# Kernel optimization log

Hardware: AMD Instinct MI355X
Metric: run time of the kernel (lower is better)

The kernel has to match this reference:

```python
import jax, jax.numpy as jnp
import numpy as np

B, S, D = 4, 2048, 512
H, DK = 8, 64
FFN = 2048
LEFT, CHUNK, RIGHT = 512, 128, 128
EPS = 1e-5


def _emformer_mask():
    # True = disallowed. Each query attends to its own chunk, LEFT keys before
    # the chunk start, and RIGHT keys after the chunk end.
    idx = jnp.arange(S)
    cs = (idx // CHUNK) * CHUNK                      # chunk start per query
    j = idx[None, :]
    allowed = (j >= cs[:, None] - LEFT) & (j < cs[:, None] + CHUNK + RIGHT)
    return jnp.broadcast_to(~allowed, (B, 1, S, S))


def _ln(x, g, b):
    m = jnp.mean(x, axis=-1, keepdims=True)
    v = jnp.var(x, axis=-1, keepdims=True)
    return (x - m) * jax.lax.rsqrt(v + EPS) * g + b


def setup_inputs() -> dict:
    key = jax.random.key(0)
    ks = jax.random.split(key, 8)
    w = lambda k, shp: jax.random.normal(k, shp, dtype=jnp.float32) * 0.02
    return {
        "x": jax.random.normal(ks[0], (B, S, D), dtype=jnp.float32),
        "mask": _emformer_mask(),
        "ln_in_g": jnp.ones((D,), jnp.float32), "ln_in_b": jnp.zeros((D,), jnp.float32),
        "wq": w(ks[1], (D, D)), "bq": jnp.zeros((D,), jnp.float32),
        "wk": w(ks[2], (D, D)), "bk": jnp.zeros((D,), jnp.float32),
        "wv": w(ks[3], (D, D)), "bv": jnp.zeros((D,), jnp.float32),
        "ln1_g": jnp.ones((D,), jnp.float32), "ln1_b": jnp.zeros((D,), jnp.float32),
        "w1": w(ks[4], (D, FFN)), "b1": jnp.zeros((FFN,), jnp.float32),
        "w2": w(ks[5], (FFN, D)), "b2": jnp.zeros((D,), jnp.float32),
        "ln2_g": jnp.ones((D,), jnp.float32), "ln2_b": jnp.zeros((D,), jnp.float32),
    }


def reference(x, mask, ln_in_g, ln_in_b, wq, bq, wk, bk, wv, bv,
              ln1_g, ln1_b, w1, b1, w2, b2, ln2_g, ln2_b):
    h = _ln(x, ln_in_g, ln_in_b)                                  # [B,S,D]
    q = (h @ wq + bq).reshape(B, S, H, DK).transpose(0, 2, 1, 3)   # [B,H,S,DK]
    k = (h @ wk + bk).reshape(B, S, H, DK).transpose(0, 2, 1, 3)
    v = (h @ wv + bv).reshape(B, S, H, DK).transpose(0, 2, 1, 3)
    scores = jnp.einsum("bhqd,bhkd->bhqk", q, k) / np.sqrt(DK).astype(np.float32)
    scores = jnp.where(mask, -jnp.inf, scores)
    probs = jax.nn.softmax(scores, axis=-1)
    probs = jnp.where(mask, 0.0, probs)                           # masked_fill after softmax
    out = jnp.einsum("bhqk,bhkd->bhqd", probs, v)
    out = out.transpose(0, 2, 1, 3).reshape(B, S, D)
    attn_out = out + h                                            # residual uses post-LN input
    o = _ln(attn_out, ln1_g, ln1_b)
    o = (o @ w1 + b1) @ w2 + b2 + attn_out                        # NOTE: no activation in source
    return _ln(o, ln2_g, ln2_b)
```

## Files before the change

kernel.cpp:

```cpp
#include <hip/hip_runtime.h>
#include <stdint.h>

#define B_ 4
#define S_ 2048
#define D_ 512
#define H_ 8
#define FFN_ 2048
#define M_ (B_*S_)

typedef unsigned short u16;
typedef __attribute__((ext_vector_type(8))) __bf16 bf16x8;
typedef __attribute__((ext_vector_type(8))) u16 u16x8;
typedef __attribute__((ext_vector_type(4))) float f32x4;

__device__ __forceinline__ u16 f2bf(float f) {
  uint32_t u = __builtin_bit_cast(uint32_t, f);
  u += 0x7FFFu + ((u >> 16) & 1u);
  return (u16)(u >> 16);
}
__device__ __forceinline__ bf16x8 ldfrag(const u16* p) {
  return __builtin_bit_cast(bf16x8, *(const u16x8*)p);
}
__device__ __forceinline__ void gld16(const void* g, void* l) {
  __builtin_amdgcn_global_load_lds(
      (const __attribute__((address_space(1))) void*)g,
      (__attribute__((address_space(3))) void*)l, 16, 0, 0);
}

__global__ __launch_bounds__(256)
void wtrans(const float* __restrict__ W, int K, int N, u16* __restrict__ Wt) {
  __shared__ float t[32][33];
  int n0 = blockIdx.x * 32, k0 = blockIdx.y * 32;
  int x = threadIdx.x, y = threadIdx.y;
#pragma unroll
  for (int r = 0; r < 4; r++) t[y + 8*r][x] = W[(size_t)(k0 + y + 8*r) * N + n0 + x];
  __syncthreads();
#pragma unroll
  for (int r = 0; r < 4; r++) Wt[(size_t)(n0 + y + 8*r) * K + k0 + x] = f2bf(t[x][y + 8*r]);
}

__global__ void bcat(const float* __restrict__ bq, const float* __restrict__ bk,
                     const float* __restrict__ bv, float* __restrict__ o) {
  int i = blockIdx.x * 256 + threadIdx.x;
  o[i] = i < 512 ? bq[i] : (i < 1024 ? bk[i - 512] : bv[i - 1024]);
}

template <bool OUT32, bool OUT16>
__global__ __launch_bounds__(128)
void ln_k(const float* __restrict__ x, const float* __restrict__ g,
          const float* __restrict__ bta, float* __restrict__ y32, u16* __restrict__ y16) {
  int row = blockIdx.x;
  int t = threadIdx.x;
  const float* xr = x + (size_t)row * 512;
  f32x4 v = *(const f32x4*)(xr + t * 4);
  float s = v.x + v.y + v.z + v.w;
  float s2 = v.x*v.x + v.y*v.y + v.z*v.z + v.w*v.w;
#pragma unroll
  for (int m = 32; m; m >>= 1) { s += __shfl_xor(s, m); s2 += __shfl_xor(s2, m); }
  __shared__ float p[4];
  int wv = t >> 6;
  if ((t & 63) == 0) { p[wv] = s; p[2 + wv] = s2; }
  __syncthreads();
  s = p[0] + p[1]; s2 = p[2] + p[3];
  float mean = s * (1.f / 512.f);
  float var = s2 * (1.f / 512.f) - mean * mean;
  float rs = rsqrtf(var + 1e-5f);
#pragma unroll
  for (int j = 0; j < 4; j++) {
    float o = (v[j] - mean) * rs * g[t*4 + j] + bta[t*4 + j];
    if constexpr (OUT32) y32[(size_t)row * 512 + t*4 + j] = o;
    if constexpr (OUT16) y16[(size_t)row * 512 + t*4 + j] = f2bf(o);
  }
}

template <int NTW, int NCOL, bool RESID, bool OUT32, bool OUT16>
__global__ __launch_bounds__(256)
void gemm_db(const u16* __restrict__ A, const u16* __restrict__ Bt,
             const float* __restrict__ bias, int K, int N,
             const float* __restrict__ resid, float* __restrict__ C32,
             u16* __restrict__ C16) {
  __shared__ __align__(16) u16 As[2][128 * 32];
  __shared__ __align__(16) u16 Bs[2][NTW * 1024];
  const int tid = threadIdx.x;
  const int wave = tid >> 6, lane = tid & 63;
  const int l15 = lane & 15, quad = lane >> 4;
  const int wm = wave >> 1, wn = wave & 1;

  const int lin = blockIdx.x;
  const int rpx = (M_ / 128) / 8;
  const int xcd = lin & 7, local = lin >> 3;
  const int row0 = (xcd * rpx + local / NCOL) * 128;
  const int col0 = (local % NCOL) * (NTW * 32);

  f32x4 acc[4][NTW];
#pragma unroll
  for (int i = 0; i < 4; i++)
#pragma unroll
    for (int j = 0; j < NTW; j++) acc[i][j] = (f32x4){0.f, 0.f, 0.f, 0.f};

  const int lr = lane >> 2;
  const int lc = ((lane & 3) ^ ((lane >> 3) & 3)) * 8;
  const u16* aG0 = A + (size_t)(row0 + (wave * 2) * 16 + lr) * K + lc;
  const u16* aG1 = A + (size_t)(row0 + (wave * 2 + 1) * 16 + lr) * K + lc;
  const int aO0 = (wave * 2) * 512 + lane * 8;
  const int aO1 = (wave * 2 + 1) * 512 + lane * 8;
  const u16* bG[NTW / 2];
  int bO[NTW / 2];
#pragma unroll
  for (int i = 0; i < NTW / 2; i++) {
    int ch = wave * (NTW / 2) + i;
    bG[i] = Bt + (size_t)(col0 + ch * 16 + lr) * K + lc;
    bO[i] = ch * 512 + lane * 8;
  }
  const int rsw = (l15 >> 1) & 3;

  gld16(aG0, &As[0][aO0]);
  gld16(aG1, &As[0][aO1]);
#pragma unroll
  for (int i = 0; i < NTW / 2; i++) gld16(bG[i], &Bs[0][bO[i]]);

  const int nIter = K >> 5;
  for (int it = 0; it < nIter; it++) {
    __syncthreads();
    const int cur = it & 1;
    if (it + 1 < nIter) {
      const int nxt = cur ^ 1;
      const int k = (it + 1) << 5;
      gld16(aG0 + k, &As[nxt][aO0]);
      gld16(aG1 + k, &As[nxt][aO1]);
#pragma unroll
      for (int i = 0; i < NTW / 2; i++) gld16(bG[i] + k, &Bs[nxt][bO[i]]);
    }
    bf16x8 af[4], bf[NTW];
#pragma unroll
    for (int mt = 0; mt < 4; mt++)
      af[mt] = ldfrag(&As[cur][(wm * 64 + mt * 16 + l15) * 32 + ((quad ^ rsw) * 8)]);
#pragma unroll
    for (int nt = 0; nt < NTW; nt++)
      bf[nt] = ldfrag(&Bs[cur][(wn * (NTW * 16) + nt * 16 + l15) * 32 + ((quad ^ rsw) * 8)]);
#pragma unroll
    for (int mt = 0; mt < 4; mt++)
#pragma unroll
      for (int nt = 0; nt < NTW; nt++)
        acc[mt][nt] = __builtin_amdgcn_mfma_f32_16x16x32_bf16(af[mt], bf[nt], acc[mt][nt], 0, 0, 0);
  }
#pragma unroll
  for (int mt = 0; mt < 4; mt++)
#pragma unroll
    for (int nt = 0; nt < NTW; nt++) {
      int n = col0 + wn * (NTW * 16) + nt * 16 + l15;
      float bv = bias[n];
#pragma unroll
      for (int r = 0; r < 4; r++) {
        int m = row0 + wm * 64 + mt * 16 + quad * 4 + r;
        float val = acc[mt][nt][r] + bv;
        if constexpr (RESID) val += resid[(size_t)m * N + n];
        if constexpr (OUT32) C32[(size_t)m * N + n] = val;
        if constexpr (OUT16) C16[(size_t)m * N + n] = f2bf(val);
      }
    }
}

__global__ __launch_bounds__(256)
void vtrans(const u16* __restrict__ qkv, u16* __restrict__ vt) {
  __shared__ u16 t[64][65];
  int s0 = blockIdx.x * 64, h = blockIdx.y, b = blockIdx.z;
  int x = threadIdx.x, y = threadIdx.y;
  const u16* src = qkv + (size_t)(b * 2048 + s0) * 1536 + 1024 + h * 64;
#pragma unroll
  for (int r = 0; r < 16; r++) { int s = y + 4*r; t[s][x] = src[(size_t)s * 1536 + x]; }
  __syncthreads();
  u16* dst = vt + (size_t)((b * 8 + h) * 64) * 2048 + s0;
#pragma unroll
  for (int r = 0; r < 16; r++) { int d = y + 4*r; dst[(size_t)d * 2048 + x] = t[x][d]; }
}

#define PSTR 136
__global__ __launch_bounds__(256)
void attn_k(const u16* __restrict__ qkv, const u16* __restrict__ vt,
            const float* __restrict__ hres, float* __restrict__ attn) {
  __shared__ __align__(16) u16 smem[8192 + 8192 + 128 * PSTR];
  u16* Ks = smem;
  u16* Vts = smem + 8192;
  u16* Ps = smem + 16384;
  u16* Qs = Ps;

  const int c = blockIdx.x, hh = blockIdx.y, b = blockIdx.z;
  const int s0 = c * 128;
  const int tid = threadIdx.x, wave = tid >> 6, lane = tid & 63;
  const int l15 = lane & 15, quad = lane >> 4;
  const int t_lo = (c > 4) ? c - 4 : 0;
  const int t_hi = (c + 2 < 16) ? c + 2 : 16;
  const int l7sw = l15 & 7;

  {
    const int cg = ((lane & 7) ^ (lane >> 3)) * 8;
    const int cp = (lane & 7) * 8;
#pragma unroll
    for (int q2 = 0; q2 < 4; q2++) {
      int r = wave * 32 + q2 * 8 + (lane >> 3);
      gld16(qkv + (size_t)(b * 2048 + s0 + r) * 1536 + hh * 64 + cg, Qs + r * 64 + cp);
    }
  }
  __syncthreads();
  bf16x8 qf[2][2];
#pragma unroll
  for (int qg = 0; qg < 2; qg++)
#pragma unroll
    for (int f = 0; f < 2; f++)
      qf[qg][f] = ldfrag(Qs + (qg * 64 + wave * 16 + l15) * 64 + (((f * 4 + quad) ^ l7sw) * 8));

  f32x4 accO[2][4];
#pragma unroll
  for (int qg = 0; qg < 2; qg++)
#pragma unroll
    for (int i = 0; i < 4; i++) accO[qg][i] = (f32x4){0.f, 0.f, 0.f, 0.f};
  float den[2][4] = {{0.f, 0.f, 0.f, 0.f}, {0.f, 0.f, 0.f, 0.f}};

  for (int kt = t_lo; kt < t_hi; ++kt) {
    __syncthreads();
    {
      const int cgk = ((lane & 7) ^ (lane >> 3)) * 8;
      const int cpk = (lane & 7) * 8;
#pragma unroll
      for (int q2 = 0; q2 < 4; q2++) {
        int r = wave * 32 + q2 * 8 + (lane >> 3);
        gld16(qkv + (size_t)(b * 2048 + kt * 128 + r) * 1536 + 512 + hh * 64 + cgk,
              Ks + r * 64 + cpk);
      }
      const int cpv = (lane & 15) * 8;
#pragma unroll
      for (int q2 = 0; q2 < 4; q2++) {
        int d = (wave * 4 + q2) * 4 + (lane >> 4);
        int cgv = ((lane & 8) | ((lane & 7) ^ (lane >> 4) ^ ((q2 & 1) << 2))) * 8;
        gld16(vt + (size_t)((b * 8 + hh) * 64 + d) * 2048 + kt * 128 + cgv,
              Vts + d * 128 + cpv);
      }
    }
    __syncthreads();

#pragma unroll
    for (int nt = 0; nt < 8; nt++) {
      bf16x8 kf0 = ldfrag(Ks + (nt * 16 + l15) * 64 + ((quad ^ l7sw) * 8));
      bf16x8 kf1 = ldfrag(Ks + (nt * 16 + l15) * 64 + (((4 + quad) ^ l7sw) * 8));
#pragma unroll
      for (int qg = 0; qg < 2; qg++) {
        f32x4 s4 = (f32x4){0.f, 0.f, 0.f, 0.f};
        s4 = __builtin_amdgcn_mfma_f32_16x16x32_bf16(qf[qg][0], kf0, s4, 0, 0, 0);
        s4 = __builtin_amdgcn_mfma_f32_16x16x32_bf16(qf[qg][1], kf1, s4, 0, 0, 0);
#pragma unroll
        for (int r = 0; r < 4; r++) {
          float pp = exp2f(s4[r] * (1.4426950408889634f * 0.125f));
          den[qg][r] += pp;
          Ps[(qg * 64 + wave * 16 + quad * 4 + r) * PSTR + nt * 16 + l15] = f2bf(pp);
        }
      }
    }
#pragma unroll
    for (int ki = 0; ki < 4; ki++) {
      bf16x8 pf[2];
#pragma unroll
      for (int qg = 0; qg < 2; qg++)
        pf[qg] = ldfrag(Ps + (qg * 64 + wave * 16 + l15) * PSTR + (ki * 4 + quad) * 8);
#pragma unroll
      for (int dt = 0; dt < 4; dt++) {
        int g = ki * 4 + quad;
        bf16x8 vf = ldfrag(Vts + (dt * 16 + l15) * 128 + (((g & 8) | ((g & 7) ^ l7sw)) * 8));
#pragma unroll
        for (int qg = 0; qg < 2; qg++)
          accO[qg][dt] = __builtin_amdgcn_mfma_f32_16x16x32_bf16(pf[qg], vf, accO[qg][dt], 0, 0, 0);
      }
    }
  }
#pragma unroll
  for (int qg = 0; qg < 2; qg++)
#pragma unroll
    for (int r = 0; r < 4; r++) {
      float d = den[qg][r];
      d += __shfl_xor(d, 1); d += __shfl_xor(d, 2);
      d += __shfl_xor(d, 4); d += __shfl_xor(d, 8);
      den[qg][r] = d;
    }
#pragma unroll
  for (int qg = 0; qg < 2; qg++)
#pragma unroll
    for (int dt = 0; dt < 4; dt++)
#pragma unroll
      for (int r = 0; r < 4; r++) {
        int m = s0 + qg * 64 + wave * 16 + quad * 4 + r;
        size_t idx = (size_t)(b * 2048 + m) * 512 + hh * 64 + dt * 16 + l15;
        attn[idx] = accO[qg][dt][r] / den[qg][r] + hres[idx];
      }
}

extern "C" void kernel_launch(void* const* d_in, const int* in_sizes, int n_in,
                              void* d_out, int out_size, void* d_ws, size_t ws_size,
                              hipStream_t stream) {
  (void)in_sizes; (void)n_in; (void)out_size; (void)ws_size;
  const float* x       = (const float*)d_in[0];
  const float* ln_in_g = (const float*)d_in[2];
  const float* ln_in_b = (const float*)d_in[3];
  const float* wq = (const float*)d_in[4];
  const float* bq = (const float*)d_in[5];
  const float* wk = (const float*)d_in[6];
  const float* bk = (const float*)d_in[7];
  const float* wv = (const float*)d_in[8];
  const float* bv = (const float*)d_in[9];
  const float* ln1_g = (const float*)d_in[10];
  const float* ln1_b = (const float*)d_in[11];
  const float* w1 = (const float*)d_in[12];
  const float* b1 = (const float*)d_in[13];
  const float* w2 = (const float*)d_in[14];
  const float* b2 = (const float*)d_in[15];
  const float* ln2_g = (const float*)d_in[16];
  const float* ln2_b = (const float*)d_in[17];

  char* ws = (char*)d_ws;
  size_t off = 0;
  auto alloc = [&](size_t bytes) {
    void* p = ws + off;
    off = (off + bytes + 255) & ~(size_t)255;
    return p;
  };
  u16*   wqkvt = (u16*)  alloc((size_t)1536 * 512 * 2);
  float* bqkv  = (float*)alloc(1536 * 4);
  u16*   w1t   = (u16*)  alloc((size_t)2048 * 512 * 2);
  u16*   w2t   = (u16*)  alloc((size_t)512 * 2048 * 2);
  float* h32   = (float*)alloc((size_t)M_ * 512 * 4);
  u16*   h16   = (u16*)  alloc((size_t)M_ * 512 * 2);
  u16*   qkv16 = (u16*)  alloc((size_t)M_ * 1536 * 2);
  u16*   vtb   = (u16*)  alloc((size_t)B_ * H_ * 64 * 2048 * 2);
  float* attn32= (float*)alloc((size_t)M_ * 512 * 4);
  float* out2  = h32;
  u16*   o16   = h16;
  u16*   f16b  = qkv16;

  wtrans<<<dim3(16, 16), dim3(32, 8), 0, stream>>>(wq, 512, 512, wqkvt);
  wtrans<<<dim3(16, 16), dim3(32, 8), 0, stream>>>(wk, 512, 512, wqkvt + (size_t)512 * 512);
  wtrans<<<dim3(16, 16), dim3(32, 8), 0, stream>>>(wv, 512, 512, wqkvt + (size_t)1024 * 512);
  wtrans<<<dim3(64, 16), dim3(32, 8), 0, stream>>>(w1, 512, 2048, w1t);
  wtrans<<<dim3(16, 64), dim3(32, 8), 0, stream>>>(w2, 2048, 512, w2t);
  bcat<<<6, 256, 0, stream>>>(bq, bk, bv, bqkv);

  ln_k<true, true><<<M_, 128, 0, stream>>>(x, ln_in_g, ln_in_b, h32, h16);
  gemm_db<4, 12, false, false, true><<<dim3(12 * 64), 256, 0, stream>>>(
      h16, wqkvt, bqkv, 512, 1536, nullptr, nullptr, qkv16);
  vtrans<<<dim3(32, 8, 4), dim3(64, 4), 0, stream>>>(qkv16, vtb);
  attn_k<<<dim3(16, 8, 4), 256, 0, stream>>>(qkv16, vtb, h32, attn32);
  ln_k<false, true><<<M_, 128, 0, stream>>>(attn32, ln1_g, ln1_b, nullptr, o16);
  gemm_db<4, 16, false, false, true><<<dim3(16 * 64), 256, 0, stream>>>(
      o16, w1t, b1, 512, 2048, nullptr, nullptr, f16b);
  gemm_db<2, 8, true, true, false><<<dim3(8 * 64), 256, 0, stream>>>(
      f16b, w2t, b2, 2048, 512, attn32, out2, nullptr);
  ln_k<true, false><<<M_, 128, 0, stream>>>(out2, ln2_g, ln2_b, (float*)d_out, nullptr);
}
```

Measured before the change: 296.2 us.

## Split attention into 64-row query tiles and split-K the final FFN GEMM

```diff
diff --git a/kernel.cpp b/kernel.cpp
--- a/kernel.cpp
+++ b/kernel.cpp
@@ -11,6 +11,7 @@
 typedef unsigned short u16;
 typedef __attribute__((ext_vector_type(8))) __bf16 bf16x8;
 typedef __attribute__((ext_vector_type(8))) u16 u16x8;
+typedef __attribute__((ext_vector_type(4))) u16 u16x4;
 typedef __attribute__((ext_vector_type(4))) float f32x4;
 
 __device__ __forceinline__ u16 f2bf(float f) {
@@ -45,14 +46,21 @@
   o[i] = i < 512 ? bq[i] : (i < 1024 ? bk[i - 512] : bv[i - 1024]);
 }
 
-template <bool OUT32, bool OUT16>
+template <bool OUT32, bool OUT16, bool SUM2>
 __global__ __launch_bounds__(128)
 void ln_k(const float* __restrict__ x, const float* __restrict__ g,
-          const float* __restrict__ bta, float* __restrict__ y32, u16* __restrict__ y16) {
+          const float* __restrict__ bta, float* __restrict__ y32,
+          u16* __restrict__ y16, const u16* __restrict__ x2) {
   int row = blockIdx.x;
   int t = threadIdx.x;
   const float* xr = x + (size_t)row * 512;
   f32x4 v = *(const f32x4*)(xr + t * 4);
+  if constexpr (SUM2) {
+    u16x4 p2 = *(const u16x4*)(x2 + (size_t)row * 512 + t * 4);
+#pragma unroll
+    for (int j = 0; j < 4; j++)
+      v[j] += __builtin_bit_cast(float, (uint32_t)p2[j] << 16);
+  }
   float s = v.x + v.y + v.z + v.w;
   float s2 = v.x*v.x + v.y*v.y + v.z*v.z + v.w*v.w;
 #pragma unroll
@@ -73,7 +81,7 @@
   }
 }
 
-template <int NTW, int NCOL, bool RESID, bool OUT32, bool OUT16>
+template <int NTW, int NCOL, int KSPLIT, bool RESID, bool OUT32, bool OUT16>
 __global__ __launch_bounds__(256)
 void gemm_db(const u16* __restrict__ A, const u16* __restrict__ Bt,
              const float* __restrict__ bias, int K, int N,
@@ -86,11 +94,19 @@
   const int l15 = lane & 15, quad = lane >> 4;
   const int wm = wave >> 1, wn = wave & 1;
 
-  const int lin = blockIdx.x;
+  int lin = blockIdx.x;
+  int kh = 0;
+  if constexpr (KSPLIT == 2) {
+    const int nblk = (M_ / 128) * NCOL;
+    kh = lin >= nblk;
+    lin -= kh * nblk;
+  }
   const int rpx = (M_ / 128) / 8;
   const int xcd = lin & 7, local = lin >> 3;
   const int row0 = (xcd * rpx + local / NCOL) * 128;
   const int col0 = (local % NCOL) * (NTW * 32);
+  const int klen = K / KSPLIT;
+  const int kstart = kh * klen;
 
   f32x4 acc[4][NTW];
 #pragma unroll
@@ -114,18 +130,18 @@
   }
   const int rsw = (l15 >> 1) & 3;
 
-  gld16(aG0, &As[0][aO0]);
-  gld16(aG1, &As[0][aO1]);
-#pragma unroll
-  for (int i = 0; i < NTW / 2; i++) gld16(bG[i], &Bs[0][bO[i]]);
-
-  const int nIter = K >> 5;
+  gld16(aG0 + kstart, &As[0][aO0]);
+  gld16(aG1 + kstart, &As[0][aO1]);
+#pragma unroll
+  for (int i = 0; i < NTW / 2; i++) gld16(bG[i] + kstart, &Bs[0][bO[i]]);
+
+  const int nIter = klen >> 5;
   for (int it = 0; it < nIter; it++) {
     __syncthreads();
     const int cur = it & 1;
     if (it + 1 < nIter) {
       const int nxt = cur ^ 1;
-      const int k = (it + 1) << 5;
+      const int k = kstart + ((it + 1) << 5);
       gld16(aG0 + k, &As[nxt][aO0]);
       gld16(aG1 + k, &As[nxt][aO1]);
 #pragma unroll
@@ -149,14 +165,21 @@
 #pragma unroll
     for (int nt = 0; nt < NTW; nt++) {
       int n = col0 + wn * (NTW * 16) + nt * 16 + l15;
-      float bv = bias[n];
+      float bv;
+      if constexpr (KSPLIT == 2) bv = (kh == 0) ? bias[n] : 0.f;
+      else bv = bias[n];
 #pragma unroll
       for (int r = 0; r < 4; r++) {
         int m = row0 + wm * 64 + mt * 16 + quad * 4 + r;
         float val = acc[mt][nt][r] + bv;
-        if constexpr (RESID) val += resid[(size_t)m * N + n];
-        if constexpr (OUT32) C32[(size_t)m * N + n] = val;
-        if constexpr (OUT16) C16[(size_t)m * N + n] = f2bf(val);
+        if constexpr (KSPLIT == 2) {
+          if (kh == 0) C32[(size_t)m * N + n] = val + resid[(size_t)m * N + n];
+          else C16[(size_t)m * N + n] = f2bf(val);
+        } else {
+          if constexpr (RESID) val += resid[(size_t)m * N + n];
+          if constexpr (OUT32) C32[(size_t)m * N + n] = val;
+          if constexpr (OUT16) C16[(size_t)m * N + n] = f2bf(val);
+        }
       }
     }
 }
@@ -179,14 +202,19 @@
 __global__ __launch_bounds__(256)
 void attn_k(const u16* __restrict__ qkv, const u16* __restrict__ vt,
             const float* __restrict__ hres, float* __restrict__ attn) {
-  __shared__ __align__(16) u16 smem[8192 + 8192 + 128 * PSTR];
+  __shared__ __align__(16) u16 smem[8192 + 8192 + 64 * PSTR];
   u16* Ks = smem;
   u16* Vts = smem + 8192;
   u16* Ps = smem + 16384;
   u16* Qs = Ps;
 
-  const int c = blockIdx.x, hh = blockIdx.y, b = blockIdx.z;
-  const int s0 = c * 128;
+  const int lin = blockIdx.x;
+  const int xcd = lin & 7, g = lin >> 3;
+  const int cq = g & 31;
+  const int bh = xcd * 4 + (g >> 5);
+  const int hh = bh & 7, b = bh >> 3;
+  const int c = cq >> 1;
+  const int s0 = cq * 64;
   const int tid = threadIdx.x, wave = tid >> 6, lane = tid & 63;
   const int l15 = lane & 15, quad = lane >> 4;
   const int t_lo = (c > 4) ? c - 4 : 0;
@@ -197,25 +225,24 @@
     const int cg = ((lane & 7) ^ (lane >> 3)) * 8;
     const int cp = (lane & 7) * 8;
 #pragma unroll
-    for (int q2 = 0; q2 < 4; q2++) {
-      int r = wave * 32 + q2 * 8 + (lane >> 3);
+    for (int q2 = 0; q2 < 2; q2++) {
+      int r = wave * 16 + q2 * 8 + (lane >> 3);
       gld16(qkv + (size_t)(b * 2048 + s0 + r) * 1536 + hh * 64 + cg, Qs + r * 64 + cp);
     }
   }
   __syncthreads();
-  bf16x8 qf[2][2];
-#pragma unroll
-  for (int qg = 0; qg < 2; qg++)
-#pragma unroll
-    for (int f = 0; f < 2; f++)
-      qf[qg][f] = ldfrag(Qs + (qg * 64 + wave * 16 + l15) * 64 + (((f * 4 + quad) ^ l7sw) * 8));
-
-  f32x4 accO[2][4];
-#pragma unroll
-  for (int qg = 0; qg < 2; qg++)
-#pragma unroll
-    for (int i = 0; i < 4; i++) accO[qg][i] = (f32x4){0.f, 0.f, 0.f, 0.f};
-  float den[2][4] = {{0.f, 0.f, 0.f, 0.f}, {0.f, 0.f, 0.f, 0.f}};
+  bf16x8 qf[2];
+#pragma unroll
+  for (int f = 0; f < 2; f++)
+    qf[f] = ldfrag(Qs + (wave * 16 + l15) * 64 + (((f * 4 + quad) ^ l7sw) * 8));
+
+  const u16x8 ones16 = {0x3F80, 0x3F80, 0x3F80, 0x3F80, 0x3F80, 0x3F80, 0x3F80, 0x3F80};
+  const bf16x8 onesf = __builtin_bit_cast(bf16x8, ones16);
+
+  f32x4 accO[4];
+#pragma unroll
+  for (int i = 0; i < 4; i++) accO[i] = (f32x4){0.f, 0.f, 0.f, 0.f};
+  f32x4 accD = (f32x4){0.f, 0.f, 0.f, 0.f};
 
   for (int kt = t_lo; kt < t_hi; ++kt) {
     __syncthreads();
@@ -243,54 +270,38 @@
     for (int nt = 0; nt < 8; nt++) {
       bf16x8 kf0 = ldfrag(Ks + (nt * 16 + l15) * 64 + ((quad ^ l7sw) * 8));
       bf16x8 kf1 = ldfrag(Ks + (nt * 16 + l15) * 64 + (((4 + quad) ^ l7sw) * 8));
-#pragma unroll
-      for (int qg = 0; qg < 2; qg++) {
-        f32x4 s4 = (f32x4){0.f, 0.f, 0.f, 0.f};
-        s4 = __builtin_amdgcn_mfma_f32_16x16x32_bf16(qf[qg][0], kf0, s4, 0, 0, 0);
-        s4 = __builtin_amdgcn_mfma_f32_16x16x32_bf16(qf[qg][1], kf1, s4, 0, 0, 0);
-#pragma unroll
-        for (int r = 0; r < 4; r++) {
-          float pp = exp2f(s4[r] * (1.4426950408889634f * 0.125f));
-          den[qg][r] += pp;
-          Ps[(qg * 64 + wave * 16 + quad * 4 + r) * PSTR + nt * 16 + l15] = f2bf(pp);
-        }
+      f32x4 s4 = (f32x4){0.f, 0.f, 0.f, 0.f};
+      s4 = __builtin_amdgcn_mfma_f32_16x16x32_bf16(qf[0], kf0, s4, 0, 0, 0);
+      s4 = __builtin_amdgcn_mfma_f32_16x16x32_bf16(qf[1], kf1, s4, 0, 0, 0);
+#pragma unroll
+      for (int r = 0; r < 4; r++) {
+        float pp = exp2f(s4[r] * (1.4426950408889634f * 0.125f));
+        Ps[(wave * 16 + quad * 4 + r) * PSTR + nt * 16 + l15] =
+            (u16)(__builtin_bit_cast(uint32_t, pp) >> 16);
       }
     }
 #pragma unroll
     for (int ki = 0; ki < 4; ki++) {
-      bf16x8 pf[2];
-#pragma unroll
-      for (int qg = 0; qg < 2; qg++)
-        pf[qg] = ldfrag(Ps + (qg * 64 + wave * 16 + l15) * PSTR + (ki * 4 + quad) * 8);
+      bf16x8 pf = ldfrag(Ps + (wave * 16 + l15) * PSTR + (ki * 4 + quad) * 8);
+      accD = __builtin_amdgcn_mfma_f32_16x16x32_bf16(pf, onesf, accD, 0, 0, 0);
 #pragma unroll
       for (int dt = 0; dt < 4; dt++) {
-        int g = ki * 4 + quad;
-        bf16x8 vf = ldfrag(Vts + (dt * 16 + l15) * 128 + (((g & 8) | ((g & 7) ^ l7sw)) * 8));
-#pragma unroll
-        for (int qg = 0; qg < 2; qg++)
-          accO[qg][dt] = __builtin_amdgcn_mfma_f32_16x16x32_bf16(pf[qg], vf, accO[qg][dt], 0, 0, 0);
-      }
-    }
-  }
-#pragma unroll
-  for (int qg = 0; qg < 2; qg++)
-#pragma unroll
-    for (int r = 0; r < 4; r++) {
-      float d = den[qg][r];
-      d += __shfl_xor(d, 1); d += __shfl_xor(d, 2);
-      d += __shfl_xor(d, 4); d += __shfl_xor(d, 8);
-      den[qg][r] = d;
-    }
-#pragma unroll
-  for (int qg = 0; qg < 2; qg++)
-#pragma unroll
-    for (int dt = 0; dt < 4; dt++)
-#pragma unroll
-      for (int r = 0; r < 4; r++) {
-        int m = s0 + qg * 64 + wave * 16 + quad * 4 + r;
-        size_t idx = (size_t)(b * 2048 + m) * 512 + hh * 64 + dt * 16 + l15;
-        attn[idx] = accO[qg][dt][r] / den[qg][r] + hres[idx];
-      }
+        int gg = ki * 4 + quad;
+        bf16x8 vf = ldfrag(Vts + (dt * 16 + l15) * 128 + (((gg & 8) | ((gg & 7) ^ l7sw)) * 8));
+        accO[dt] = __builtin_amdgcn_mfma_f32_16x16x32_bf16(pf, vf, accO[dt], 0, 0, 0);
+      }
+    }
+  }
+#pragma unroll
+  for (int r = 0; r < 4; r++) {
+    float dinv = 1.0f / accD[r];
+    int m = s0 + wave * 16 + quad * 4 + r;
+#pragma unroll
+    for (int dt = 0; dt < 4; dt++) {
+      size_t idx = (size_t)(b * 2048 + m) * 512 + hh * 64 + dt * 16 + l15;
+      attn[idx] = accO[dt][r] * dinv + hres[idx];
+    }
+  }
 }
 
 extern "C" void kernel_launch(void* const* d_in, const int* in_sizes, int n_in,
@@ -342,15 +353,15 @@
   wtrans<<<dim3(16, 64), dim3(32, 8), 0, stream>>>(w2, 2048, 512, w2t);
   bcat<<<6, 256, 0, stream>>>(bq, bk, bv, bqkv);
 
-  ln_k<true, true><<<M_, 128, 0, stream>>>(x, ln_in_g, ln_in_b, h32, h16);
-  gemm_db<4, 12, false, false, true><<<dim3(12 * 64), 256, 0, stream>>>(
+  ln_k<true, true, false><<<M_, 128, 0, stream>>>(x, ln_in_g, ln_in_b, h32, h16, nullptr);
+  gemm_db<4, 12, 1, false, false, true><<<dim3(12 * 64), 256, 0, stream>>>(
       h16, wqkvt, bqkv, 512, 1536, nullptr, nullptr, qkv16);
   vtrans<<<dim3(32, 8, 4), dim3(64, 4), 0, stream>>>(qkv16, vtb);
-  attn_k<<<dim3(16, 8, 4), 256, 0, stream>>>(qkv16, vtb, h32, attn32);
-  ln_k<false, true><<<M_, 128, 0, stream>>>(attn32, ln1_g, ln1_b, nullptr, o16);
-  gemm_db<4, 16, false, false, true><<<dim3(16 * 64), 256, 0, stream>>>(
+  attn_k<<<dim3(1024), 256, 0, stream>>>(qkv16, vtb, h32, attn32);
+  ln_k<false, true, false><<<M_, 128, 0, stream>>>(attn32, ln1_g, ln1_b, nullptr, o16, nullptr);
+  gemm_db<4, 16, 1, false, false, true><<<dim3(16 * 64), 256, 0, stream>>>(
       o16, w1t, b1, 512, 2048, nullptr, nullptr, f16b);
-  gemm_db<2, 8, true, true, false><<<dim3(8 * 64), 256, 0, stream>>>(
-      f16b, w2t, b2, 2048, 512, attn32, out2, nullptr);
-  ln_k<true, false><<<M_, 128, 0, stream>>>(out2, ln2_g, ln2_b, (float*)d_out, nullptr);
-}
+  gemm_db<2, 8, 2, false, false, false><<<dim3(2 * 8 * 64), 256, 0, stream>>>(
+      f16b, w2t, b2, 2048, 512, attn32, out2, h16);
+  ln_k<true, false, true><<<M_, 128, 0, stream>>>(out2, ln2_g, ln2_b, (float*)d_out, nullptr, h16);
+}
```

After: 296.2 us. No clear change (-0.0%).
